# Kernel tuning notes

Hardware: AMD Instinct MI355X
Metric: run time of the kernel (lower is better)

## Reference

```python
import jax, jax.numpy as jnp
import numpy as np

NUM_LAYERS = 2
SHAPES = [(100, 100), (50, 50), (25, 25), (13, 13)]  # (H, W) per level
D, NH, NP, NL = 256, 8, 4, 4
DH = D // NH
DFF = 1024
B = 2
S = sum(h * w for h, w in SHAPES)  # 13294


def layer_norm(x, g, b, eps=1e-5):
    m = x.mean(-1, keepdims=True)
    v = jnp.var(x, axis=-1, keepdims=True)
    return (x - m) * jax.lax.rsqrt(v + eps) * g + b


def get_reference_points(valid_ratios):
    refs = []
    for lvl, (H_, W_) in enumerate(SHAPES):
        ry, rx = jnp.meshgrid(jnp.linspace(0.5, H_ - 0.5, H_),
                              jnp.linspace(0.5, W_ - 0.5, W_), indexing='ij')
        ry = ry.reshape(-1)[None] / (valid_ratios[:, None, lvl, 1] * H_)
        rx = rx.reshape(-1)[None] / (valid_ratios[:, None, lvl, 0] * W_)
        refs.append(jnp.stack([rx, ry], -1))
    ref = jnp.concatenate(refs, 1)                      # [B, S, 2]
    return ref[:, :, None] * valid_ratios[:, None]      # [B, S, NL, 2]


def sample_level(value_l, H_, W_, loc):
    # value_l: [B, nH, H*W, Dh]; loc: [B, Q, nH, P, 2] normalized in [0,1]
    x = loc[..., 0] * W_ - 0.5
    y = loc[..., 1] * H_ - 0.5
    x0 = jnp.floor(x)
    y0 = jnp.floor(y)
    Bq, Q = loc.shape[0], loc.shape[1]
    acc = 0.
    corners = ((x0, y0, (x0 + 1 - x) * (y0 + 1 - y)),
               (x0 + 1, y0, (x - x0) * (y0 + 1 - y)),
               (x0, y0 + 1, (x0 + 1 - x) * (y - y0)),
               (x0 + 1, y0 + 1, (x - x0) * (y - y0)))
    for xi, yi, w in corners:  # zero-padding grid_sample: invalid corners contribute 0
        valid = (xi >= 0) & (xi <= W_ - 1) & (yi >= 0) & (yi <= H_ - 1)
        idx = (jnp.clip(yi, 0, H_ - 1) * W_ + jnp.clip(xi, 0, W_ - 1)).astype(jnp.int32)
        idx = jnp.transpose(idx, (0, 2, 1, 3)).reshape(Bq, NH, Q * NP)
        g = jnp.take_along_axis(value_l, idx[..., None], axis=2)  # [B,nH,Q*P,Dh]
        wv = jnp.transpose((w * valid).astype(value_l.dtype), (0, 2, 1, 3)).reshape(Bq, NH, Q * NP)
        acc = acc + g * wv[..., None]
    return acc.reshape(Bq, NH, Q, NP, DH)


def msda(query, ref, src, W_val, b_val, W_off, b_off, W_attn, b_attn, W_out, b_out):
    Bq, Q = query.shape[:2]
    value = (src @ W_val + b_val).reshape(Bq, S, NH, DH)
    off = (query @ W_off + b_off).reshape(Bq, Q, NH, NL, NP, 2)
    attn = jax.nn.softmax((query @ W_attn + b_attn).reshape(Bq, Q, NH, NL * NP), -1)
    attn = attn.reshape(Bq, Q, NH, NL, NP)
    normalizer = jnp.array([[w, h] for h, w in SHAPES], dtype=query.dtype)  # [NL,2] (x,y)
    loc = ref[:, :, None, :, None, :] + off / normalizer[None, None, None, :, None, :]
    out = jnp.zeros((Bq, NH, Q, DH), query.dtype)
    start = 0
    for l, (H_, W_) in enumerate(SHAPES):
        v_l = jnp.transpose(value[:, start:start + H_ * W_], (0, 2, 1, 3))  # [B,nH,HW,Dh]
        samp = sample_level(v_l, H_, W_, loc[:, :, :, l])                    # [B,nH,Q,P,Dh]
        w_l = jnp.transpose(attn[:, :, :, l], (0, 2, 1, 3))                  # [B,nH,Q,P]
        out = out + (samp * w_l[..., None]).sum(3)
        start += H_ * W_
    out = jnp.transpose(out, (0, 2, 1, 3)).reshape(Bq, Q, D)
    return out @ W_out + b_out


def setup_inputs() -> dict:
    key = jax.random.key(0)
    ks = jax.random.split(key, 12)
    sc = 0.02
    inp = {
        'src': jax.random.normal(ks[0], (B, S, D), jnp.float32),
        'spatial_shapes': np.array(SHAPES, dtype=np.int64),
        'valid_ratios': jnp.ones((B, NL, 2), jnp.float32),
        'W_off': sc * jax.random.normal(ks[1], (NUM_LAYERS, D, NH * NL * NP * 2), jnp.float32),
        'b_off': jnp.zeros((NUM_LAYERS, NH * NL * NP * 2), jnp.float32),
        'W_attn': sc * jax.random.normal(ks[2], (NUM_LAYERS, D, NH * NL * NP), jnp.float32),
        'b_attn': jnp.zeros((NUM_LAYERS, NH * NL * NP), jnp.float32),
        'W_val': sc * jax.random.normal(ks[3], (NUM_LAYERS, D, D), jnp.float32),
        'b_val': jnp.zeros((NUM_LAYERS, D), jnp.float32),
        'W_out': sc * jax.random.normal(ks[4], (NUM_LAYERS, D, D), jnp.float32),
        'b_out': jnp.zeros((NUM_LAYERS, D), jnp.float32),
        'ln1_g': jnp.ones((NUM_LAYERS, D), jnp.float32),
        'ln1_b': jnp.zeros((NUM_LAYERS, D), jnp.float32),
        'W1': sc * jax.random.normal(ks[5], (NUM_LAYERS, D, DFF), jnp.float32),
        'b1': jnp.zeros((NUM_LAYERS, DFF), jnp.float32),
        'W2': sc * jax.random.normal(ks[6], (NUM_LAYERS, DFF, D), jnp.float32),
        'b2': jnp.zeros((NUM_LAYERS, D), jnp.float32),
        'ln2_g': jnp.ones((NUM_LAYERS, D), jnp.float32),
        'ln2_b': jnp.zeros((NUM_LAYERS, D), jnp.float32),
    }
    return inp


def reference(src, spatial_shapes, valid_ratios, W_off, b_off, W_attn, b_attn,
              W_val, b_val, W_out, b_out, ln1_g, ln1_b, W1, b1, W2, b2, ln2_g, ln2_b):
    # Deformable-DETR encoder stack (dropout=0 / eval mode, pos=None, no padding mask).
    ref = get_reference_points(valid_ratios)  # [B, S, NL, 2]
    x = src
    for i in range(NUM_LAYERS):
        x2 = msda(x, ref, x, W_val[i], b_val[i], W_off[i], b_off[i],
                  W_attn[i], b_attn[i], W_out[i], b_out[i])
        x = layer_norm(x + x2, ln1_g[i], ln1_b[i])
        h = jax.nn.relu(x @ W1[i] + b1[i]) @ W2[i] + b2[i]
        x = layer_norm(x + h, ln2_g[i], ln2_b[i])
    return x
```

## Files before the change

### kernel.cpp

```cpp
#include <hip/hip_runtime.h>
#include <math.h>


#define S_TOT 13294
#define BATCH 2
#define M_TOT (BATCH * S_TOT)
#define M_PAD 26624

typedef __attribute__((ext_vector_type(8))) short short8;
typedef __attribute__((ext_vector_type(4))) float floatx4;
typedef __attribute__((ext_vector_type(2))) float floatx2;

#define AS1C(p) ((const __attribute__((address_space(1))) void*)(p))
#define AS3(p)  ((__attribute__((address_space(3))) void*)(p))

static __device__ __forceinline__ unsigned short f2bf(float x) {
    union { float f; unsigned u; } v; v.f = x;
    unsigned r = v.u + 0x7FFFu + ((v.u >> 16) & 1u);
    return (unsigned short)(r >> 16);
}
static __device__ __forceinline__ float b2f(unsigned short u) {
    union { unsigned u; float f; } v; v.u = (unsigned)u << 16; return v.f;
}
static __device__ __forceinline__ float bflo(unsigned u) {
    union { unsigned u; float f; } v; v.u = u << 16; return v.f;
}
static __device__ __forceinline__ float bfhi(unsigned u) {
    union { unsigned u; float f; } v; v.u = u & 0xFFFF0000u; return v.f;
}
static __device__ __forceinline__ float braw(unsigned u) {
    union { unsigned u; float f; } v; v.u = u; return v.f;
}

template<int TM, bool RELU, bool BF16OUT, bool PROJ>
__global__ __launch_bounds__(256)
void mgemm(const unsigned short* __restrict__ A,
           const unsigned short* __restrict__ BT,
           const float* __restrict__ bias,
           const float* __restrict__ bias2,
           const float* __restrict__ bias3,
           unsigned short* __restrict__ Cb,
           unsigned short* __restrict__ Cb2,
           int M, int N, int K)
{
    constexpr int WM = (TM == 128) ? 2 : 1;
    constexpr int WN = 4 / WM;
    constexpr int MI = TM / (WM * 16);
    constexpr int NI = 128 / (WN * 16);
    __shared__ __align__(16) unsigned short smemA[2 * TM * 32];
    __shared__ __align__(16) unsigned short smemB[2 * 128 * 32];
    const int tid  = threadIdx.x;
    const int lane = tid & 63;
    const int w    = tid >> 6;
    const int wm   = w % WM, wn = w / WM;
    const int lr   = lane & 15, quad = lane >> 4;
    const int bm   = blockIdx.y * TM;
    const int bn   = blockIdx.x * 128;

    floatx4 acc[MI][NI];
    #pragma unroll
    for (int i = 0; i < MI; ++i)
        #pragma unroll
        for (int j = 0; j < NI; ++j)
            acc[i][j] = (floatx4){0.f, 0.f, 0.f, 0.f};

    const int srow = lane >> 2;
    const int selt = (lane & 3) << 3;

    for (int k0 = 0; k0 < K; k0 += 64) {
        #pragma unroll
        for (int c = 0; c < 2; ++c) {
            if (TM == 128) {
                #pragma unroll
                for (int jj = 0; jj < 2; ++jj) {
                    const int j = 2 * w + jj;
                    const unsigned short* ga = A  + (size_t)(bm + j * 16 + srow) * K + k0 + c * 32 + selt;
                    const unsigned short* gb = BT + (size_t)(bn + j * 16 + srow) * K + k0 + c * 32 + selt;
                    __builtin_amdgcn_global_load_lds(AS1C(ga), AS3(smemA + c * (TM * 32) + j * 512), 16, 0, 0);
                    __builtin_amdgcn_global_load_lds(AS1C(gb), AS3(smemB + c * 4096 + j * 512), 16, 0, 0);
                }
            } else {
                const unsigned short* ga = A + (size_t)(bm + w * 16 + srow) * K + k0 + c * 32 + selt;
                __builtin_amdgcn_global_load_lds(AS1C(ga), AS3(smemA + c * (TM * 32) + w * 512), 16, 0, 0);
                #pragma unroll
                for (int jj = 0; jj < 2; ++jj) {
                    const int j = 2 * w + jj;
                    const unsigned short* gb = BT + (size_t)(bn + j * 16 + srow) * K + k0 + c * 32 + selt;
                    __builtin_amdgcn_global_load_lds(AS1C(gb), AS3(smemB + c * 4096 + j * 512), 16, 0, 0);
                }
            }
        }
        __syncthreads();

        #pragma unroll
        for (int c = 0; c < 2; ++c) {
            short8 av[MI], bv[NI];
            #pragma unroll
            for (int mi = 0; mi < MI; ++mi)
                av[mi] = *(const short8*)&smemA[c * (TM * 32) + (wm * MI * 16 + mi * 16 + lr) * 32 + quad * 8];
            #pragma unroll
            for (int ni = 0; ni < NI; ++ni)
                bv[ni] = *(const short8*)&smemB[c * 4096 + (wn * NI * 16 + ni * 16 + lr) * 32 + quad * 8];
            #pragma unroll
            for (int mi = 0; mi < MI; ++mi)
                #pragma unroll
                for (int ni = 0; ni < NI; ++ni)
                    acc[mi][ni] = __builtin_amdgcn_mfma_f32_16x16x32_bf16(
                        av[mi], bv[ni], acc[mi][ni], 0, 0, 0);
        }
        __syncthreads();
    }

    #pragma unroll
    for (int mi = 0; mi < MI; ++mi) {
        #pragma unroll
        for (int ni = 0; ni < NI; ++ni) {
            #pragma unroll
            for (int r = 0; r < 4; ++r) {
                const int row = bm + wm * MI * 16 + mi * 16 + quad * 4 + r;
                const int col = bn + wn * NI * 16 + ni * 16 + lr;
                if (PROJ) {
                    const float bb = (col < 256) ? bias[col]
                                   : (col < 512) ? bias2[col - 256]
                                                 : bias3[col - 512];
                    const float v = acc[mi][ni][r] + bb;
                    if (col < 256) Cb[(size_t)row * 256 + col] = f2bf(v);
                    else           Cb2[(size_t)row * 384 + (col - 256)] = f2bf(v);
                } else {
                    float v = acc[mi][ni][r] + bias[col];
                    if (RELU) v = fmaxf(v, 0.0f);
                    if (BF16OUT) Cb[(size_t)row * N + col] = f2bf(v);
                }
            }
        }
    }
}

template<bool HASF, bool HASB>
__global__ __launch_bounds__(512)
void mgemm_ln(const unsigned short* __restrict__ A,
              const unsigned short* __restrict__ BT,
              const float* __restrict__ bias,
              const unsigned short* __restrict__ R,
              const float* __restrict__ g,
              const float* __restrict__ beta,
              float* __restrict__ outF,
              unsigned short* __restrict__ outB,
              int M, int K)
{
    __shared__ __align__(16) unsigned short smemA[4096];
    __shared__ __align__(16) unsigned short smemB[16384];
    const int lane = threadIdx.x & 63;
    const int w    = threadIdx.x >> 6;
    const int lr   = lane & 15, quad = lane >> 4;
    const int bm   = blockIdx.x * 64;
    const int srow = lane >> 2;
    const int sw   = (((lane & 3) ^ (srow & 3)) << 3);

    floatx4 acc[4][2];
    #pragma unroll
    for (int i = 0; i < 4; ++i)
        #pragma unroll
        for (int j = 0; j < 2; ++j)
            acc[i][j] = (floatx4){0.f, 0.f, 0.f, 0.f};

    const int NK = K >> 6;
    for (int kt = 0; kt < NK; ++kt) {
        const int k0 = kt << 6;
        {
            const int c = w & 1, j = w >> 1;
            const unsigned short* ga = A + (size_t)(bm + j * 16 + srow) * K + k0 + c * 32 + sw;
            __builtin_amdgcn_global_load_lds(AS1C(ga), AS3(smemA + c * 2048 + j * 512), 16, 0, 0);
        }
        #pragma unroll
        for (int c = 0; c < 2; ++c) {
            #pragma unroll
            for (int jj = 0; jj < 2; ++jj) {
                const int j = w * 2 + jj;
                const unsigned short* gb = BT + (size_t)(j * 16 + srow) * K + k0 + c * 32 + sw;
                __builtin_amdgcn_global_load_lds(AS1C(gb), AS3(smemB + c * 8192 + j * 512), 16, 0, 0);
            }
        }
        __syncthreads();

        #pragma unroll
        for (int c = 0; c < 2; ++c) {
            short8 av[4], bv[2];
            #pragma unroll
            for (int mi = 0; mi < 4; ++mi) {
                const int row = mi * 16 + lr;
                av[mi] = *(const short8*)&smemA[c * 2048 + row * 32 + ((quad ^ (row & 3)) << 3)];
            }
            #pragma unroll
            for (int ni = 0; ni < 2; ++ni) {
                const int col = w * 32 + ni * 16 + lr;
                bv[ni] = *(const short8*)&smemB[c * 8192 + col * 32 + ((quad ^ (col & 3)) << 3)];
            }
            #pragma unroll
            for (int mi = 0; mi < 4; ++mi)
                #pragma unroll
                for (int ni = 0; ni < 2; ++ni)
                    acc[mi][ni] = __builtin_amdgcn_mfma_f32_16x16x32_bf16(
                        av[mi], bv[ni], acc[mi][ni], 0, 0, 0);
        }
        __syncthreads();
    }

    float bs[2], gs[2], bts[2];
    #pragma unroll
    for (int ni = 0; ni < 2; ++ni) {
        const int col = w * 32 + ni * 16 + lr;
        bs[ni] = bias[col]; gs[ni] = g[col]; bts[ni] = beta[col];
    }
    float* lnbuf = (float*)smemA;

    #pragma unroll
    for (int mi = 0; mi < 4; ++mi) {
        #pragma unroll
        for (int r = 0; r < 4; ++r) {
            const int rl = mi * 16 + quad * 4 + r;
            const int grow = bm + rl;
            const bool act = grow < M;
            float p = 0.f, q = 0.f;
            #pragma unroll
            for (int ni = 0; ni < 2; ++ni) {
                const int col = w * 32 + ni * 16 + lr;
                const float rv = act ? b2f(R[(size_t)grow * 256 + col]) : 0.f;
                const float x = acc[mi][ni][r] + bs[ni] + rv;
                acc[mi][ni][r] = x;
                p += x; q += x * x;
            }
            #pragma unroll
            for (int o = 1; o < 16; o <<= 1) {
                p += __shfl_xor(p, o, 64);
                q += __shfl_xor(q, o, 64);
            }
            if (lr == 0) {
                lnbuf[rl * 16 + 2 * w]     = p;
                lnbuf[rl * 16 + 2 * w + 1] = q;
            }
        }
    }
    __syncthreads();
    #pragma unroll
    for (int mi = 0; mi < 4; ++mi) {
        #pragma unroll
        for (int r = 0; r < 4; ++r) {
            const int rl = mi * 16 + quad * 4 + r;
            const int grow = bm + rl;
            const float4 pa = *(const float4*)&lnbuf[rl * 16];
            const float4 pb = *(const float4*)&lnbuf[rl * 16 + 4];
            const float4 pc = *(const float4*)&lnbuf[rl * 16 + 8];
            const float4 pd = *(const float4*)&lnbuf[rl * 16 + 12];
            const float s  = pa.x + pa.z + pb.x + pb.z + pc.x + pc.z + pd.x + pd.z;
            const float s2 = pa.y + pa.w + pb.y + pb.w + pc.y + pc.w + pd.y + pd.w;
            const float mean = s * (1.0f / 256.0f);
            const float var  = s2 * (1.0f / 256.0f) - mean * mean;
            const float rs   = rsqrtf(var + 1e-5f);
            if (grow < M) {
                #pragma unroll
                for (int ni = 0; ni < 2; ++ni) {
                    const int col = w * 32 + ni * 16 + lr;
                    const float y = (acc[mi][ni][r] - mean) * rs * gs[ni] + bts[ni];
                    if (HASF) outF[(size_t)grow * 256 + col] = y;
                    if (HASB) outB[(size_t)grow * 256 + col] = f2bf(y);
                }
            }
        }
    }
}

__global__ __launch_bounds__(256)
void convpad(const float* __restrict__ X, unsigned short* __restrict__ Y, int M)
{
    const int idx = blockIdx.x * 256 + threadIdx.x;
    const int row = idx >> 6;
    const int c4  = (idx & 63) << 2;
    if (row >= M_PAD) return;
    float4 v = {0.f, 0.f, 0.f, 0.f};
    if (row < M) v = ((const float4*)(X + (size_t)row * 256))[c4 >> 2];
    unsigned p0 = (unsigned)f2bf(v.x) | ((unsigned)f2bf(v.y) << 16);
    unsigned p1 = (unsigned)f2bf(v.z) | ((unsigned)f2bf(v.w) << 16);
    uint2 o; o.x = p0; o.y = p1;
    *(uint2*)(Y + (size_t)row * 256 + c4) = o;
}

struct WJobs {
    const float* W[12];
    unsigned short* WT[12];
    int K[12], N[12], tx[12], start[12];
};

__global__ __launch_bounds__(256)
void wtrans_all(WJobs jb)
{
    __shared__ float t[32][33];
    const int bx = blockIdx.x;
    int seg = 0;
    #pragma unroll
    for (int s = 1; s < 12; ++s) if (bx >= jb.start[s]) seg = s;
    const float* W = jb.W[seg];
    unsigned short* WT = jb.WT[seg];
    const int K = jb.K[seg], N = jb.N[seg], tx = jb.tx[seg];
    const int local = bx - jb.start[seg];
    const int n0 = (local % tx) * 32, k0 = (local / tx) * 32;
    const int c = threadIdx.x & 31, r0 = threadIdx.x >> 5;
    #pragma unroll
    for (int rr = r0; rr < 32; rr += 8)
        t[rr][c] = W[(size_t)(k0 + rr) * N + n0 + c];
    __syncthreads();
    #pragma unroll
    for (int rr = r0; rr < 32; rr += 8)
        WT[(size_t)(n0 + rr) * K + k0 + c] = f2bf(t[c][rr]);
}

__global__ __launch_bounds__(256)
void msda_kernel(const unsigned short* __restrict__ valb,
                 const unsigned short* __restrict__ oab,
                 const float* __restrict__ vr,
                 unsigned short* __restrict__ out)
{
    __shared__ __align__(16) char smeta[8 * 128 * 32];
    const int t = threadIdx.x;
    const int bid = (blockIdx.x & 7) * 416 + (blockIdx.x >> 3);

    {
        const int wv = t >> 6, lane = t & 63;
        const int lqA = wv * 2 + (lane >> 5);
        const int bq = bid * 8 + lqA;
        const int h = (lane >> 2) & 7;
        const int j = lane & 3;
        if (bq < M_TOT) {
            const int b = (bq >= S_TOT) ? 1 : 0;
            const int q = bq - b * S_TOT;
            const int bofs = b * (S_TOT * 512);
            int Hq, rr, cc, lq;
            if (q < 10000)      { lq = 0; Hq = 100; rr = q / 100;              cc = q - rr * 100; }
            else if (q < 12500) { lq = 1; Hq = 50;  int r2 = q - 10000; rr = r2 / 50; cc = r2 - rr * 50; }
            else if (q < 13125) { lq = 2; Hq = 25;  int r2 = q - 12500; rr = r2 / 25; cc = r2 - rr * 25; }
            else                { lq = 3; Hq = 13;  int r2 = q - 13125; rr = r2 / 13; cc = r2 - rr * 13; }
            const float rxb = (cc + 0.5f) / (vr[(b * 4 + lq) * 2 + 0] * (float)Hq);
            const float ryb = (rr + 0.5f) / (vr[(b * 4 + lq) * 2 + 1] * (float)Hq);
            const int HWt[4] = {100, 50, 25, 13};
            const int stt[4] = {0, 10000, 12500, 13125};
            const int HW = HWt[j], st = stt[j];
            const float fW = (float)HW;
            const float refxw = rxb * vr[(b * 4 + j) * 2 + 0] * fW - 0.5f;
            const float refyw = ryb * vr[(b * 4 + j) * 2 + 1] * fW - 0.5f;
            const unsigned short* row = oab + (size_t)bq * 384;
            const uint2 lgu = *(const uint2*)(row + 256 + h * 16 + j * 4);
            const float l0 = bflo(lgu.x), l1 = bfhi(lgu.x);
            const float l2 = bflo(lgu.y), l3 = bfhi(lgu.y);
            float mx = fmaxf(fmaxf(l0, l1), fmaxf(l2, l3));
            mx = fmaxf(mx, __shfl_xor(mx, 1, 64));
            mx = fmaxf(mx, __shfl_xor(mx, 2, 64));
            const float e0 = __expf(l0 - mx), e1 = __expf(l1 - mx);
            const float e2 = __expf(l2 - mx), e3 = __expf(l3 - mx);
            float ss = e0 + e1 + e2 + e3;
            ss += __shfl_xor(ss, 1, 64);
            ss += __shfl_xor(ss, 2, 64);
            const float inv = 1.0f / ss;
            const uint4 ou = *(const uint4*)(row + h * 32 + j * 8);
            const float oxs[4] = {bflo(ou.x), bflo(ou.y), bflo(ou.z), bflo(ou.w)};
            const float oys[4] = {bfhi(ou.x), bfhi(ou.y), bfhi(ou.z), bfhi(ou.w)};
            const float aw[4]  = {e0 * inv, e1 * inv, e2 * inv, e3 * inv};
            char* mb = smeta + (size_t)(lqA * 128 + h * 16 + j * 4) * 32;
            const int swz = ((h * 4 + j) & 7) << 4;
            #pragma unroll
            for (int p = 0; p < 4; ++p) {
                const float x = refxw + oxs[p];
                const float y = refyw + oys[p];
                const float x0f = floorf(x), y0f = floorf(y);
                const int x0 = (int)x0f, y0 = (int)y0f;
                const float fx = x - x0f, fy = y - y0f;
                const float wb[4] = {(1.f - fx) * (1.f - fy), fx * (1.f - fy),
                                     (1.f - fx) * fy,         fx * fy};
                const int xs[2] = {x0, x0 + 1};
                const int ys2[2] = {y0, y0 + 1};
                int iv[4]; float wv4[4];
                #pragma unroll
                for (int k = 0; k < 4; ++k) {
                    const int xi = xs[k & 1], yi = ys2[k >> 1];
                    const bool vld = ((unsigned)xi < (unsigned)HW) && ((unsigned)yi < (unsigned)HW);
                    const int xc = min(max(xi, 0), HW - 1);
                    const int yc = min(max(yi, 0), HW - 1);
                    iv[k] = bofs + ((st + yc * HW + xc) << 9) + (h << 6);
                    wv4[k] = vld ? wb[k] * aw[p] : 0.0f;
                }
                int4 i4; i4.x = iv[0]; i4.y = iv[1]; i4.z = iv[2]; i4.w = iv[3];
                float4 w4; w4.x = wv4[0]; w4.y = wv4[1]; w4.z = wv4[2]; w4.w = wv4[3];
                *(int4*)(mb + ((p * 32) ^ swz)) = i4;
                *(float4*)(mb + ((p * 32 + 16) ^ swz)) = w4;
            }
        }
    }
    __syncthreads();
    {
        const int lq2 = t >> 5;
        const int r = t & 31;
        const int h2 = r >> 2;
        const int cg = r & 3;
        const int bq2 = bid * 8 + lq2;
        if (bq2 < M_TOT) {
            const char* vbase = (const char*)valb;
            const unsigned cgo = cg * 16;
            floatx2 a0 = {0.f, 0.f}, a1 = {0.f, 0.f}, a2 = {0.f, 0.f}, a3 = {0.f, 0.f};
            const char* mb2 = smeta + (size_t)(lq2 * 128 + h2 * 16) * 32;
            #pragma unroll 4
            for (int s = 0; s < 16; ++s) {
                const int swz2 = ((h2 * 4 + (s >> 2)) & 7) << 4;
                const int4  iv = *(const int4*)(mb2 + ((s * 32) ^ swz2));
                const float4 w4 = *(const float4*)(mb2 + ((s * 32 + 16) ^ swz2));
                const uint4 u0 = *(const uint4*)(vbase + (unsigned)(iv.x + cgo));
                const uint4 u1 = *(const uint4*)(vbase + (unsigned)(iv.y + cgo));
                const uint4 u2 = *(const uint4*)(vbase + (unsigned)(iv.z + cgo));
                const uint4 u3 = *(const uint4*)(vbase + (unsigned)(iv.w + cgo));
                #define ACC8(UU, WW) { \
                    const floatx2 w2 = {WW, WW}; \
                    const floatx2 t0 = {bflo(UU.x), braw(UU.x)}; \
                    const floatx2 t1 = {bflo(UU.y), braw(UU.y)}; \
                    const floatx2 t2 = {bflo(UU.z), braw(UU.z)}; \
                    const floatx2 t3 = {bflo(UU.w), braw(UU.w)}; \
                    a0 += w2 * t0; a1 += w2 * t1; a2 += w2 * t2; a3 += w2 * t3; }
                ACC8(u0, w4.x) ACC8(u1, w4.y) ACC8(u2, w4.z) ACC8(u3, w4.w)
                #undef ACC8
            }
            uint4 o;
            o.x = (unsigned)f2bf(a0.x) | ((unsigned)f2bf(a0.y) << 16);
            o.y = (unsigned)f2bf(a1.x) | ((unsigned)f2bf(a1.y) << 16);
            o.z = (unsigned)f2bf(a2.x) | ((unsigned)f2bf(a2.y) << 16);
            o.w = (unsigned)f2bf(a3.x) | ((unsigned)f2bf(a3.y) << 16);
            *(uint4*)(out + (size_t)bq2 * 256 + h2 * 32 + cg * 8) = o;
        }
    }
}

extern "C" void kernel_launch(void* const* d_in, const int* in_sizes, int n_in,
                              void* d_out, int out_size, void* d_ws, size_t ws_size,
                              hipStream_t stream)
{
    const float* src    = (const float*)d_in[0];
    const float* vr     = (const float*)d_in[2];
    const float* W_off  = (const float*)d_in[3];
    const float* b_off  = (const float*)d_in[4];
    const float* W_attn = (const float*)d_in[5];
    const float* b_attn = (const float*)d_in[6];
    const float* W_val  = (const float*)d_in[7];
    const float* b_val  = (const float*)d_in[8];
    const float* W_out  = (const float*)d_in[9];
    const float* b_out  = (const float*)d_in[10];
    const float* ln1_g  = (const float*)d_in[11];
    const float* ln1_b  = (const float*)d_in[12];
    const float* W1     = (const float*)d_in[13];
    const float* b1     = (const float*)d_in[14];
    const float* W2     = (const float*)d_in[15];
    const float* b2     = (const float*)d_in[16];
    const float* ln2_g  = (const float*)d_in[17];
    const float* ln2_b  = (const float*)d_in[18];
    float* out = (float*)d_out;

    const int M = M_TOT;

    char* wsb = (char*)d_ws;
    unsigned short* HBF  = (unsigned short*)wsb;
    unsigned short* OAB  = (unsigned short*)wsb;
    unsigned short* VALB = (unsigned short*)(wsb + 20447232);
    unsigned short* X1B  = (unsigned short*)(wsb + 54525952);
    unsigned short* RB   = (unsigned short*)(wsb + 81788928);
    unsigned short* YBF  = (unsigned short*)(wsb + 95420416);
    unsigned short* WT   = (unsigned short*)(wsb + 109051904);

    const size_t LWT = 753664;
    const size_t oProj = 0, oOut = 163840, oW1 = 229376, oW2 = 491520;

    WJobs jb;
    int startAcc = 0;
    for (int i = 0; i < 2; ++i) {
        unsigned short* wt = WT + i * LWT;
        const float* srcs[6] = {W_val + i * 65536, W_off + i * 65536, W_attn + i * 32768,
                                W_out + i * 65536, W1 + i * 262144, W2 + i * 262144};
        unsigned short* dsts[6] = {wt + oProj, wt + oProj + 65536, wt + oProj + 131072,
                                   wt + oOut, wt + oW1, wt + oW2};
        const int Ks[6] = {256, 256, 256, 256, 256, 1024};
        const int Ns[6] = {256, 256, 128, 256, 1024, 256};
        for (int s = 0; s < 6; ++s) {
            const int idx = i * 6 + s;
            jb.W[idx] = srcs[s]; jb.WT[idx] = dsts[s];
            jb.K[idx] = Ks[s]; jb.N[idx] = Ns[s]; jb.tx[idx] = Ns[s] / 32;
            jb.start[idx] = startAcc;
            startAcc += (Ns[s] / 32) * (Ks[s] / 32);
        }
    }
    wtrans_all<<<dim3(startAcc), 256, 0, stream>>>(jb);

    const int GM128 = M_PAD / 128;
    const int GM64  = M_PAD / 64;
    const dim3 blk(256);
    const dim3 blk512(512);

    for (int i = 0; i < 2; ++i) {
        unsigned short* wt = WT + i * LWT;

        if (i == 0)
            convpad<<<dim3(M_PAD / 4), blk, 0, stream>>>(src, RB, M);

        mgemm<64, false, false, true><<<dim3(5, GM64), blk, 0, stream>>>(
            RB, wt + oProj, b_val + i * 256, b_off + i * 256, b_attn + i * 128,
            VALB, OAB, M, 640, 256);

        msda_kernel<<<dim3(3328), blk, 0, stream>>>(VALB, OAB, vr, YBF);

        mgemm_ln<false, true><<<dim3(GM64), blk512, 0, stream>>>(
            YBF, wt + oOut, b_out + i * 256, RB,
            ln1_g + i * 256, ln1_b + i * 256, nullptr, X1B, M, 256);

        mgemm<128, true, true, false><<<dim3(8, GM128), blk, 0, stream>>>(
            X1B, wt + oW1, b1 + i * 1024, nullptr, nullptr,
            HBF, nullptr, M, 1024, 256);

        if (i == 0)
            mgemm_ln<false, true><<<dim3(GM64), blk512, 0, stream>>>(
                HBF, wt + oW2, b2 + i * 256, X1B,
                ln2_g + i * 256, ln2_b + i * 256, nullptr, RB, M, 1024);
        else
            mgemm_ln<true, false><<<dim3(GM64), blk512, 0, stream>>>(
                HBF, wt + oW2, b2 + i * 256, X1B,
                ln2_g + i * 256, ln2_b + i * 256, out, nullptr, M, 1024);
    }
}
```

Before: 431.0 us.

## Load GEMM-LN operands directly into registers with double buffering, drop LDS staging

The fused GEMM+LayerNorm kernel stops staging A and B tiles through shared memory with global_load_lds and barriers. Each lane now loads its MFMA fragments straight from global memory into registers, prefetching the next K tile while the current one is multiplied. The residual loads for the epilogue are hoisted ahead of the reduction. This removes LDS traffic and two barriers per K step. In exchange, B is reloaded redundantly across blocks, the A rows are read with strided uncoalesced accesses, and register pressure rises.

```diff
diff --git a/kernel.cpp b/kernel.cpp
--- a/kernel.cpp
+++ b/kernel.cpp
@@ -148,14 +148,11 @@
               unsigned short* __restrict__ outB,
               int M, int K)
 {
-    __shared__ __align__(16) unsigned short smemA[4096];
-    __shared__ __align__(16) unsigned short smemB[16384];
+    __shared__ float lnbuf[64 * 16];
     const int lane = threadIdx.x & 63;
     const int w    = threadIdx.x >> 6;
     const int lr   = lane & 15, quad = lane >> 4;
     const int bm   = blockIdx.x * 64;
-    const int srow = lane >> 2;
-    const int sw   = (((lane & 3) ^ (srow & 3)) << 3);
 
     floatx4 acc[4][2];
     #pragma unroll
@@ -164,46 +161,58 @@
         for (int j = 0; j < 2; ++j)
             acc[i][j] = (floatx4){0.f, 0.f, 0.f, 0.f};
 
+    const unsigned short* ap[4];
+    const unsigned short* bp[2];
+    #pragma unroll
+    for (int mi = 0; mi < 4; ++mi)
+        ap[mi] = A + (size_t)(bm + mi * 16 + lr) * K + quad * 8;
+    #pragma unroll
+    for (int ni = 0; ni < 2; ++ni)
+        bp[ni] = BT + (size_t)(w * 32 + ni * 16 + lr) * K + quad * 8;
+
     const int NK = K >> 6;
+
+    short8 a0[4][2], b0[2][2];
+    #pragma unroll
+    for (int c = 0; c < 2; ++c) {
+        #pragma unroll
+        for (int mi = 0; mi < 4; ++mi)
+            a0[mi][c] = *(const short8*)(ap[mi] + c * 32);
+        #pragma unroll
+        for (int ni = 0; ni < 2; ++ni)
+            b0[ni][c] = *(const short8*)(bp[ni] + c * 32);
+    }
     for (int kt = 0; kt < NK; ++kt) {
-        const int k0 = kt << 6;
-        {
-            const int c = w & 1, j = w >> 1;
-            const unsigned short* ga = A + (size_t)(bm + j * 16 + srow) * K + k0 + c * 32 + sw;
-            __builtin_amdgcn_global_load_lds(AS1C(ga), AS3(smemA + c * 2048 + j * 512), 16, 0, 0);
-        }
-        #pragma unroll
-        for (int c = 0; c < 2; ++c) {
-            #pragma unroll
-            for (int jj = 0; jj < 2; ++jj) {
-                const int j = w * 2 + jj;
-                const unsigned short* gb = BT + (size_t)(j * 16 + srow) * K + k0 + c * 32 + sw;
-                __builtin_amdgcn_global_load_lds(AS1C(gb), AS3(smemB + c * 8192 + j * 512), 16, 0, 0);
-            }
-        }
-        __syncthreads();
-
-        #pragma unroll
-        for (int c = 0; c < 2; ++c) {
-            short8 av[4], bv[2];
-            #pragma unroll
-            for (int mi = 0; mi < 4; ++mi) {
-                const int row = mi * 16 + lr;
-                av[mi] = *(const short8*)&smemA[c * 2048 + row * 32 + ((quad ^ (row & 3)) << 3)];
-            }
-            #pragma unroll
-            for (int ni = 0; ni < 2; ++ni) {
-                const int col = w * 32 + ni * 16 + lr;
-                bv[ni] = *(const short8*)&smemB[c * 8192 + col * 32 + ((quad ^ (col & 3)) << 3)];
-            }
+        short8 a1[4][2], b1[2][2];
+        if (kt + 1 < NK) {
+            const int k1 = (kt + 1) << 6;
+            #pragma unroll
+            for (int c = 0; c < 2; ++c) {
+                #pragma unroll
+                for (int mi = 0; mi < 4; ++mi)
+                    a1[mi][c] = *(const short8*)(ap[mi] + k1 + c * 32);
+                #pragma unroll
+                for (int ni = 0; ni < 2; ++ni)
+                    b1[ni][c] = *(const short8*)(bp[ni] + k1 + c * 32);
+            }
+        }
+        #pragma unroll
+        for (int c = 0; c < 2; ++c)
             #pragma unroll
             for (int mi = 0; mi < 4; ++mi)
                 #pragma unroll
                 for (int ni = 0; ni < 2; ++ni)
                     acc[mi][ni] = __builtin_amdgcn_mfma_f32_16x16x32_bf16(
-                        av[mi], bv[ni], acc[mi][ni], 0, 0, 0);
-        }
-        __syncthreads();
+                        a0[mi][c], b0[ni][c], acc[mi][ni], 0, 0, 0);
+        if (kt + 1 < NK) {
+            #pragma unroll
+            for (int c = 0; c < 2; ++c) {
+                #pragma unroll
+                for (int mi = 0; mi < 4; ++mi) a0[mi][c] = a1[mi][c];
+                #pragma unroll
+                for (int ni = 0; ni < 2; ++ni) b0[ni][c] = b1[ni][c];
+            }
+        }
     }
 
     float bs[2], gs[2], bts[2];
@@ -212,21 +221,31 @@
         const int col = w * 32 + ni * 16 + lr;
         bs[ni] = bias[col]; gs[ni] = g[col]; bts[ni] = beta[col];
     }
-    float* lnbuf = (float*)smemA;
+
+    unsigned short rv[4][4][2];
+    #pragma unroll
+    for (int mi = 0; mi < 4; ++mi) {
+        #pragma unroll
+        for (int r = 0; r < 4; ++r) {
+            const int grow = bm + mi * 16 + quad * 4 + r;
+            const bool act = grow < M;
+            #pragma unroll
+            for (int ni = 0; ni < 2; ++ni) {
+                const int col = w * 32 + ni * 16 + lr;
+                rv[mi][r][ni] = act ? R[(size_t)grow * 256 + col] : (unsigned short)0;
+            }
+        }
+    }
 
     #pragma unroll
     for (int mi = 0; mi < 4; ++mi) {
         #pragma unroll
         for (int r = 0; r < 4; ++r) {
             const int rl = mi * 16 + quad * 4 + r;
-            const int grow = bm + rl;
-            const bool act = grow < M;
             float p = 0.f, q = 0.f;
             #pragma unroll
             for (int ni = 0; ni < 2; ++ni) {
-                const int col = w * 32 + ni * 16 + lr;
-                const float rv = act ? b2f(R[(size_t)grow * 256 + col]) : 0.f;
-                const float x = acc[mi][ni][r] + bs[ni] + rv;
+                const float x = acc[mi][ni][r] + bs[ni] + b2f(rv[mi][r][ni]);
                 acc[mi][ni][r] = x;
                 p += x; q += x * x;
             }
```

Result: slower. 614.2 us (+42.5%).
